# Performance work log

Measured on AMD Instinct MI355X. Metric: run time of the kernel, lower is better.

The kernel has to match this reference:

```python
import jax, jax.numpy as jnp
import numpy as np

EMBED_DIM = 512
NHEAD = 8
HEAD_DIM = EMBED_DIM // NHEAD
NEG_INF = -1e8
U, B, R, S, M = 1024, 16, 256, 32, 31
Q = R + U + S   # 1312
KV = M + R + U  # 1311


def setup_inputs() -> dict:
    key = jax.random.key(0)
    ks = jax.random.split(key, 12)
    f = lambda k, shp: jax.random.normal(k, shp, dtype=jnp.float32)
    s = 1.0 / np.sqrt(EMBED_DIM)
    return {
        "utterance": f(ks[0], (U, B, EMBED_DIM)),
        "right_context": f(ks[1], (R, B, EMBED_DIM)),
        "summary": f(ks[2], (S, B, EMBED_DIM)),
        "memory": f(ks[3], (M, B, EMBED_DIM)),
        "attention_mask": jax.random.randint(ks[4], (Q, KV), 0, 2).astype(bool),
        "padding_mask": jax.random.randint(ks[5], (B, KV), 0, 2).astype(bool),
        "Wq": f(ks[6], (EMBED_DIM, EMBED_DIM)) * s,
        "bq": f(ks[7], (EMBED_DIM,)) * 0.1,
        "Wkv": f(ks[8], (2 * EMBED_DIM, EMBED_DIM)) * s,
        "bkv": f(ks[9], (2 * EMBED_DIM,)) * 0.1,
        "Wo": f(ks[10], (EMBED_DIM, EMBED_DIM)) * s * 0.25,
        "bo": f(ks[11], (EMBED_DIM,)) * 0.1,
    }


def reference(utterance, right_context, summary, memory, attention_mask,
              padding_mask, Wq, bq, Wkv, bkv, Wo, bo):
    scaling = HEAD_DIM ** -0.5
    # query = [right_context, utterance, summary]  -> (Q, B, D)
    q_in = jnp.concatenate([right_context, utterance, summary], axis=0)
    # key/value = [memory, right_context, utterance] -> (KV, B, D)
    kv_in = jnp.concatenate([memory, right_context, utterance], axis=0)
    query = q_in @ Wq.T + bq
    kv = kv_in @ Wkv.T + bkv
    key_t, value = jnp.split(kv, 2, axis=2)

    def heads(t):  # (L, B, D) -> (B*nhead, L, head_dim)
        return t.reshape(t.shape[0], B * NHEAD, HEAD_DIM).transpose(1, 0, 2)

    qh = heads(query) * scaling
    kh = heads(key_t)
    vh = heads(value)
    # (B*nhead, Q, KV) attention scores in float32 (matches .float() cast)
    w = jnp.einsum('bqd,bkd->bqk', qh, kh).astype(jnp.float32)
    w = jnp.where(attention_mask[None], NEG_INF, w)
    w = w.reshape(B, NHEAD, Q, KV)
    w = jnp.where(padding_mask[:, None, None, :], NEG_INF, w)
    probs = jax.nn.softmax(w.reshape(B * NHEAD, Q, KV), axis=-1)
    # dropout p=0.0 -> identity
    attn = jnp.einsum('bqk,bkd->bqd', probs, vh)  # (B*nhead, Q, head_dim)
    attn = attn.transpose(1, 0, 2).reshape(Q, B, EMBED_DIM)
    out = attn @ Wo.T + bo
    output_right_context_utterance = out[:R + U]
    # tanh_on_mem=False -> clamp to [-10, 10]; forward returns memory[:-1]
    output_memory = jnp.clip(out[R + U:], -10.0, 10.0)[:-1]
    return output_right_context_utterance, output_memory
```

## Files before the change

### kernel.cpp

```cpp
#include <hip/hip_runtime.h>
#include <hip/hip_bf16.h>

#define EMBED 512
#define NHEAD 8
#define HDIM  64
#define B_    16
#define U_    1024
#define R_    256
#define S_    32
#define M_    31
#define Q_    (R_ + U_ + S_)
#define KV_   (M_ + R_ + U_)

#define QROWS  (Q_ * B_)
#define KVROWS (KV_ * B_)
#define OROWS  (1311 * B_)
#define OUT0_ROWS (1280 * B_)

#define KVPAD_ROWS 1344
#define KPAD 1344
#define MROWSTRIDE 44

#define QSCALE 0.18033688011112042f
#define SOFF  16.0f
#define MASKV (-40.0f)

typedef __attribute__((ext_vector_type(8))) short bf16x8;
typedef __attribute__((ext_vector_type(4))) short short4v;
typedef __attribute__((ext_vector_type(4))) float f32x4;
#define MFMA16(a, b, c) __builtin_amdgcn_mfma_f32_16x16x32_bf16(a, b, c, 0, 0, 0)

typedef unsigned short ushort_t;

__device__ __forceinline__ ushort_t f2bf(float x) {
    __hip_bfloat16 h = __float2bfloat16(x);
    return *reinterpret_cast<ushort_t*>(&h);
}
__device__ __forceinline__ float bf2f(ushort_t h) {
    return __uint_as_float((unsigned)h << 16);
}
__device__ __forceinline__ float exp2_raw(float x) {
    return __builtin_amdgcn_exp2f(x);
}

__device__ __forceinline__ void gload_lds16(const void* g, void* l) {
    __builtin_amdgcn_global_load_lds(
        (const __attribute__((address_space(1))) unsigned int*)g,
        (__attribute__((address_space(3))) unsigned int*)l, 16, 0, 0);
}

__global__ __launch_bounds__(256) void cvt_all(
    const float* __restrict__ s0, const float* __restrict__ s1,
    const float* __restrict__ s2, const float* __restrict__ s3,
    const float* __restrict__ s4, const float* __restrict__ s5,
    const float* __restrict__ s6,
    ushort_t* __restrict__ SRC_hi, ushort_t* __restrict__ SRC_lo,
    ushort_t* __restrict__ W_hi,  ushort_t* __restrict__ W_lo,
    const int* __restrict__ am, const int* __restrict__ pm,
    unsigned* __restrict__ am_p, unsigned* __restrict__ pm_p)
{
    int bid = blockIdx.x;
    if (bid >= 5884) {
        const int NA = Q_ * MROWSTRIDE;
        const int NP = B_ * MROWSTRIDE;
        int idx = (bid - 5884) * 256 + threadIdx.x;
        if (idx < NA) {
            int q = idx / MROWSTRIDE, w_ = idx % MROWSTRIDE;
            unsigned bits = 0xFFFFFFFFu;
            if (w_ < 41) {
                bits = 0;
                #pragma unroll 4
                for (int i = 0; i < 32; ++i) {
                    int kg = w_ * 32 + i;
                    int v = (kg < KV_) ? am[(size_t)q * KV_ + kg] : 1;
                    bits |= (unsigned)(v != 0) << i;
                }
            }
            am_p[idx] = bits;
        } else if (idx < NA + NP) {
            int j = idx - NA;
            int bb = j / MROWSTRIDE, w_ = j % MROWSTRIDE;
            unsigned bits = 0xFFFFFFFFu;
            if (w_ < 41) {
                bits = 0;
                #pragma unroll 4
                for (int i = 0; i < 32; ++i) {
                    int kg = w_ * 32 + i;
                    int v = (kg < KV_) ? pm[bb * KV_ + kg] : 1;
                    bits |= (unsigned)(v != 0) << i;
                }
            }
            pm_p[j] = bits;
        }
        return;
    }

    const float* src; ushort_t* hi; ushort_t* lo; int n8;
    if (bid < 4096)      { src = s0; hi = SRC_hi;            lo = SRC_lo;            n8 = 1048576; }
    else if (bid < 5120) { src = s1; hi = SRC_hi + 8388608;  lo = SRC_lo + 8388608;  n8 = 262144; bid -= 4096; }
    else if (bid < 5248) { src = s2; hi = SRC_hi + 10485760; lo = SRC_lo + 10485760; n8 = 32768;  bid -= 5120; }
    else if (bid < 5372) { src = s3; hi = SRC_hi + 10747904; lo = SRC_lo + 10747904; n8 = 31744;  bid -= 5248; }
    else if (bid < 5500) { src = s4; hi = W_hi;              lo = W_lo;              n8 = 32768;  bid -= 5372; }
    else if (bid < 5756) { src = s5; hi = W_hi + 262144;     lo = W_lo + 262144;     n8 = 65536;  bid -= 5500; }
    else                 { src = s6; hi = W_hi + 786432;     lo = W_lo + 786432;     n8 = 32768;  bid -= 5756; }

    int i = bid * 256 + threadIdx.x;
    if (i >= n8) return;
    const float4* s = (const float4*)(src + (size_t)i * 8);
    float4 a = s[0], b2 = s[1];
    float xs[8] = {a.x, a.y, a.z, a.w, b2.x, b2.y, b2.z, b2.w};
    bf16x8 hv, lv;
    #pragma unroll
    for (int j = 0; j < 8; ++j) {
        ushort_t hb = f2bf(xs[j]);
        hv[j] = (short)hb;
        lv[j] = (short)f2bf(xs[j] - bf2f(hb));
    }
    *(bf16x8*)(hi + (size_t)i * 8) = hv;
    *(bf16x8*)(lo + (size_t)i * 8) = lv;
}

__global__ __launch_bounds__(256) void vtrans(
    const ushort_t* __restrict__ Vp, ushort_t* __restrict__ VT)
{
    __shared__ ushort_t Lt[64][72];
    const int tid = threadIdx.x;
    const int kt  = blockIdx.x;
    const int bh  = blockIdx.y;
    const int b   = bh >> 3, h = bh & 7;
    const int sub = tid >> 3;
    const int g   = tid & 7;

    #pragma unroll
    for (int p = 0; p < 2; ++p) {
        int k = kt * 64 + p * 32 + sub;
        bf16x8 v;
        if (k < KV_) {
            v = *(const bf16x8*)(Vp + ((size_t)k * B_ + b) * EMBED + h * HDIM + g * 8);
        } else {
            #pragma unroll
            for (int j = 0; j < 8; ++j) v[j] = 0;
        }
        #pragma unroll
        for (int j = 0; j < 8; ++j)
            Lt[g * 8 + j][p * 32 + sub] = (ushort_t)v[j];
    }
    __syncthreads();
    #pragma unroll
    for (int p = 0; p < 2; ++p) {
        int d = p * 32 + sub;
        bf16x8 v = *(const bf16x8*)&Lt[d][g * 8];
        *(bf16x8*)(VT + ((size_t)(bh * 64 + d)) * KPAD + kt * 64 + g * 8) = v;
    }
}

template<int MODE>
__global__ __launch_bounds__(256) void gemm_mfma(
    const ushort_t* __restrict__ Ahi, const ushort_t* __restrict__ Alo,
    const ushort_t* __restrict__ Whi,
    const float* __restrict__ bias, float scale,
    int n0, int n01, int nrows,
    size_t off0, size_t off1, size_t off2,
    void* __restrict__ o0, void* __restrict__ o1, void* __restrict__ o2)
{
    constexpr int TERMS = (MODE == 1) ? 1 : 2;
    __shared__ __align__(16) ushort_t lAhi[128][64];
    __shared__ __align__(16) ushort_t lAlo[(TERMS == 2) ? 128 : 1][64];
    __shared__ __align__(16) ushort_t lWhi[128][64];

    const int tid = threadIdx.x;
    const int w   = tid >> 6;
    const int l   = tid & 63;
    const int l15 = l & 15;
    const int l4  = l >> 4;
    const int row0 = blockIdx.x * 128;
    const int col0 = blockIdx.y * 128;

    const int drow = l >> 3;
    const int sgr  = (l & 7) ^ drow;
    const ushort_t* aptr[4];
    const ushort_t* wptr[4];
    #pragma unroll
    for (int c = 0; c < 4; ++c) {
        int r = row0 + w * 32 + c * 8 + drow;
        int rc = r < nrows ? r : nrows - 1;
        size_t roff;
        if (MODE == 2)      roff = (size_t)rc * EMBED;
        else if (rc < n0)   roff = off0 + (size_t)rc * EMBED;
        else if (rc < n01)  roff = off1 + (size_t)(rc - n0) * EMBED;
        else                roff = off2 + (size_t)(rc - n01) * EMBED;
        aptr[c] = Ahi + roff + sgr * 8;
        int wr = col0 + w * 32 + c * 8 + drow;
        wptr[c] = Whi + (size_t)wr * EMBED + sgr * 8;
    }
    const ptrdiff_t dA = Alo - Ahi;

    f32x4 acc[4][4];
    #pragma unroll
    for (int mi = 0; mi < 4; ++mi)
        #pragma unroll
        for (int nj = 0; nj < 4; ++nj) acc[mi][nj] = (f32x4){0.f, 0.f, 0.f, 0.f};

    const int wrow = (w >> 1) * 64;
    const int wcol = (w & 1) * 64;

    for (int t = 0; t < 8; ++t) {
        __syncthreads();
        const int ke = t * 64;
        #pragma unroll
        for (int c = 0; c < 4; ++c) {
            gload_lds16(aptr[c] + ke, &lAhi[w * 32 + c * 8][0]);
            if (TERMS == 2)
                gload_lds16(aptr[c] + ke + dA, &lAlo[w * 32 + c * 8][0]);
            gload_lds16(wptr[c] + ke, &lWhi[w * 32 + c * 8][0]);
        }
        __syncthreads();

        #pragma unroll
        for (int kk = 0; kk < 2; ++kk) {
            bf16x8 ah[4], al_[4], wh[4];
            #pragma unroll
            for (int mi = 0; mi < 4; ++mi) {
                int row = wrow + mi * 16 + l15;
                int g = (((kk * 4 + l4) ^ (l15 & 7))) * 8;
                ah[mi] = *(const bf16x8*)&lAhi[row][g];
                if (TERMS == 2) al_[mi] = *(const bf16x8*)&lAlo[row][g];
            }
            #pragma unroll
            for (int nj = 0; nj < 4; ++nj) {
                int row = wcol + nj * 16 + l15;
                int g = (((kk * 4 + l4) ^ (l15 & 7))) * 8;
                wh[nj] = *(const bf16x8*)&lWhi[row][g];
            }
            #pragma unroll
            for (int mi = 0; mi < 4; ++mi)
                #pragma unroll
                for (int nj = 0; nj < 4; ++nj) {
                    acc[mi][nj] = MFMA16(ah[mi], wh[nj], acc[mi][nj]);
                    if (TERMS == 2)
                        acc[mi][nj] = MFMA16(al_[mi], wh[nj], acc[mi][nj]);
                }
        }
    }

    #pragma unroll
    for (int nj = 0; nj < 4; ++nj) {
        int gc = col0 + wcol + nj * 16 + l15;
        float bv = bias[gc];
        #pragma unroll
        for (int mi = 0; mi < 4; ++mi) {
            #pragma unroll
            for (int r = 0; r < 4; ++r) {
                int gr = row0 + wrow + mi * 16 + l4 * 4 + r;
                if (gr >= nrows) continue;
                float v = (acc[mi][nj][r] + bv) * scale;
                if (MODE == 0) {
                    ushort_t hb = f2bf(v);
                    ((ushort_t*)o0)[(size_t)gr * EMBED + gc] = hb;
                    ((ushort_t*)o1)[(size_t)gr * EMBED + gc] = f2bf(v - bf2f(hb));
                } else if (MODE == 1) {
                    if (gc < EMBED)
                        ((ushort_t*)o0)[(size_t)gr * EMBED + gc] = f2bf(v);
                    else
                        ((ushort_t*)o2)[(size_t)gr * EMBED + (gc - EMBED)] = f2bf(v);
                } else {
                    if (gr < OUT0_ROWS)
                        ((float*)o0)[(size_t)gr * EMBED + gc] = v;
                    else if (gr < OROWS)
                        ((float*)o1)[(size_t)(gr - OUT0_ROWS) * EMBED + gc] =
                            fminf(fmaxf(v, -10.f), 10.f);
                }
            }
        }
    }
}

__global__ __launch_bounds__(512, 4) void attn_mfma(
    const ushort_t* __restrict__ Qhi_p, const ushort_t* __restrict__ Qlo_p,
    const ushort_t* __restrict__ Khi_p, const ushort_t* __restrict__ VT,
    const unsigned* __restrict__ am_p, const unsigned* __restrict__ pm_p,
    ushort_t* __restrict__ Chi_p, ushort_t* __restrict__ Clo_p)
{
    __shared__ __align__(16) ushort_t Kl[2][64][64];
    __shared__ __align__(16) ushort_t Vt[2][64][64];
    __shared__ __align__(16) ushort_t Pb[8][16][72];

    const int tid = threadIdx.x;
    const int w   = tid >> 6;
    const int l   = tid & 63;
    const int l15 = l & 15;
    const int l4  = l >> 4;
    const int q0  = blockIdx.x * 128;
    const int bh  = blockIdx.y;
    const int b   = bh >> 3, h = bh & 7;

    bf16x8 Qhi[2], Qlo[2];
    {
        int qa = q0 + w * 16 + l15;
        if (qa >= Q_) qa = Q_ - 1;
        size_t base = ((size_t)qa * B_ + b) * EMBED + h * HDIM;
        #pragma unroll
        for (int dh = 0; dh < 2; ++dh) {
            Qhi[dh] = *(const bf16x8*)(Qhi_p + base + dh * 32 + l4 * 8);
            Qlo[dh] = *(const bf16x8*)(Qlo_p + base + dh * 32 + l4 * 8);
        }
    }

    bf16x8 ONES;
    #pragma unroll
    for (int j = 0; j < 8; ++j) ONES[j] = (l15 == 0) ? (short)0x3F80 : (short)0;

    const unsigned* awp;
    {
        int q = q0 + w * 16 + l15;
        if (q >= Q_) q = Q_ - 1;
        awp = am_p + (size_t)q * MROWSTRIDE;
    }
    const unsigned* pwp = pm_p + b * MROWSTRIDE;

    const int krl  = l >> 3;
    const int gsrc = (l & 7) ^ krl;
    const int srow = w * 8 + krl;

    const ushort_t* kSrc0 =
        Khi_p + ((size_t)srow * B_ + b) * EMBED + h * HDIM + gsrc * 8;
    const ushort_t* vSrc0 =
        VT + ((size_t)(bh * 64 + srow)) * KPAD + gsrc * 8;

    f32x4 SS = (f32x4){0.f, 0.f, 0.f, 0.f};
    f32x4 O[4];
    #pragma unroll
    for (int dg = 0; dg < 4; ++dg) O[dg] = (f32x4){0.f, 0.f, 0.f, 0.f};

    auto stage = [&](int kbase, int buf) {
        gload_lds16(kSrc0 + (size_t)kbase * B_ * EMBED, &Kl[buf][w * 8][0]);
        gload_lds16(vSrc0 + kbase, &Vt[buf][w * 8][0]);
    };

    stage(0, 0);
    __syncthreads();
    int cur = 0;

    for (int kt = 0; kt < 21; ++kt) {
        uint2 pw  = *(const uint2*)&pwp[2 * kt];
        uint2 awv = *(const uint2*)&awp[2 * kt];
        unsigned m0 = (awv.x | pw.x) >> (l4 * 4);
        unsigned m1 = (awv.y | pw.y) >> (l4 * 4);

        if (kt < 20) stage((kt + 1) * 64, cur ^ 1);

        f32x4 S[4];
        __builtin_amdgcn_s_setprio(1);
        #pragma unroll
        for (int c = 0; c < 4; ++c) {
            f32x4 acc = (f32x4){0.f, 0.f, 0.f, 0.f};
            int krow = c * 16 + l15;
            #pragma unroll
            for (int dh = 0; dh < 2; ++dh) {
                int gr = ((dh * 4 + l4) ^ (krow & 7)) * 8;
                bf16x8 Bh = *(const bf16x8*)&Kl[cur][krow][gr];
                acc = MFMA16(Bh, Qhi[dh], acc);
                acc = MFMA16(Bh, Qlo[dh], acc);
            }
            S[c] = acc;
        }
        __builtin_amdgcn_s_setprio(0);

        #pragma unroll
        for (int c = 0; c < 4; ++c) {
            unsigned mw = (c & 2) ? m1 : m0;
            int sh = (c & 1) << 4;
            short4v pk;
            #pragma unroll
            for (int r = 0; r < 4; ++r) {
                float s = ((mw >> (sh + r)) & 1) ? MASKV : S[c][r];
                pk[r] = (short)f2bf(exp2_raw(s - SOFF));
            }
            *(short4v*)&Pb[w][l15][c * 16 + l4 * 4] = pk;
        }

        bf16x8 PA[2];
        #pragma unroll
        for (int kh = 0; kh < 2; ++kh)
            PA[kh] = *(const bf16x8*)&Pb[w][l15][kh * 32 + l4 * 8];

        __builtin_amdgcn_s_setprio(1);
        SS = MFMA16(PA[0], ONES, SS);
        SS = MFMA16(PA[1], ONES, SS);
        #pragma unroll
        for (int kh = 0; kh < 2; ++kh)
            #pragma unroll
            for (int dg = 0; dg < 4; ++dg) {
                int vcb = ((kh * 4 + l4) ^ (l15 & 7)) << 3;
                bf16x8 VB = *(const bf16x8*)&Vt[cur][dg * 16 + l15][vcb];
                O[dg] = MFMA16(PA[kh], VB, O[dg]);
            }
        __builtin_amdgcn_s_setprio(0);

        __syncthreads();
        cur ^= 1;
    }

    #pragma unroll
    for (int r = 0; r < 4; ++r) {
        int qd = q0 + w * 16 + l4 * 4 + r;
        if (qd >= Q_) continue;
        float sT = __shfl(SS[r], l & 48, 64);
        float inv = 1.f / sT;
        #pragma unroll
        for (int dg = 0; dg < 4; ++dg) {
            float v = O[dg][r] * inv;
            size_t off = ((size_t)qd * B_ + b) * EMBED + h * HDIM + dg * 16 + l15;
            ushort_t hb = f2bf(v);
            Chi_p[off] = hb;
            Clo_p[off] = f2bf(v - bf2f(hb));
        }
    }
}

extern "C" void kernel_launch(void* const* d_in, const int* in_sizes, int n_in,
                              void* d_out, int out_size, void* d_ws, size_t ws_size,
                              hipStream_t stream) {
    const float* utter = (const float*)d_in[0];
    const float* rctx  = (const float*)d_in[1];
    const float* summ  = (const float*)d_in[2];
    const float* mem   = (const float*)d_in[3];
    const int* amask   = (const int*)d_in[4];
    const int* pmask   = (const int*)d_in[5];
    const float* Wq  = (const float*)d_in[6];
    const float* bq  = (const float*)d_in[7];
    const float* Wkv = (const float*)d_in[8];
    const float* bkv = (const float*)d_in[9];
    const float* Wo  = (const float*)d_in[10];
    const float* bo  = (const float*)d_in[11];

    const size_t UT_OFF = 0;
    const size_t RC_OFF = 8388608;
    const size_t SM_OFF = 10485760;
    const size_t MM_OFF = 10747904;
    const size_t SRC_N  = 11001856;
    const size_t WQ_OFF = 0, WKV_OFF = 262144, WO_OFF = 786432;
    const size_t W_N = 1048576;
    const size_t KVPLANE = (size_t)KVPAD_ROWS * B_ * EMBED;

    ushort_t* p = (ushort_t*)d_ws;
    ushort_t* SRC_hi = p;                p += SRC_N;
    ushort_t* SRC_lo = p;                p += SRC_N;
    ushort_t* Wp_hi  = p;                p += W_N;
    ushort_t* Wp_lo  = p;                p += W_N;
    ushort_t* Qhi_p  = p;                p += (size_t)QROWS * EMBED;
    ushort_t* Qlo_p  = p;                p += (size_t)QROWS * EMBED;
    ushort_t* Khi_p  = p;                p += KVPLANE;
    ushort_t* VT_p   = p;                p += KVPLANE;
    ushort_t* Vp     = p;                p += KVPLANE;
    ushort_t* Chi_p  = p;                p += (size_t)QROWS * EMBED;
    ushort_t* Clo_p  = p;                p += (size_t)QROWS * EMBED;
    unsigned* am_p   = (unsigned*)p;     p += (size_t)2 * KVPAD_ROWS * MROWSTRIDE;
    unsigned* pm_p   = (unsigned*)p;     p += (size_t)2 * B_ * MROWSTRIDE;

    float* out0 = (float*)d_out;
    float* out1 = out0 + (size_t)OUT0_ROWS * EMBED;

    dim3 blk(256);

    cvt_all<<<dim3(6113), blk, 0, stream>>>(
        utter, rctx, summ, mem, Wq, Wkv, Wo,
        SRC_hi, SRC_lo, Wp_hi, Wp_lo,
        amask, pmask, am_p, pm_p);

    gemm_mfma<0><<<dim3(QROWS / 128, EMBED / 128), blk, 0, stream>>>(
        SRC_hi, SRC_lo, Wp_hi + WQ_OFF, bq, QSCALE,
        R_ * B_, (R_ + U_) * B_, QROWS, RC_OFF, UT_OFF, SM_OFF,
        Qhi_p, Qlo_p, nullptr);

    gemm_mfma<1><<<dim3((KVROWS + 127) / 128, (2 * EMBED) / 128), blk, 0, stream>>>(
        SRC_hi, SRC_lo, Wp_hi + WKV_OFF, bkv, 1.0f,
        M_ * B_, (M_ + R_) * B_, KVROWS, MM_OFF, RC_OFF, UT_OFF,
        Khi_p, nullptr, Vp);

    vtrans<<<dim3(21, 128), blk, 0, stream>>>(Vp, VT_p);

    attn_mfma<<<dim3((Q_ + 127) / 128, B_ * NHEAD), dim3(512), 0, stream>>>(
        Qhi_p, Qlo_p, Khi_p, VT_p, am_p, pm_p, Chi_p, Clo_p);

    gemm_mfma<2><<<dim3(QROWS / 128, EMBED / 128), blk, 0, stream>>>(
        Chi_p, Clo_p, Wp_hi + WO_OFF, bo, 1.0f,
        QROWS, QROWS, QROWS, 0, 0, 0,
        out0, out1, nullptr);
}
```

Baseline: 334.1 us.

## Keep attention probabilities in registers by transposing MFMA operand roles

The attention kernel no longer writes the softmax probabilities to shared memory and reads them back. It swaps the MFMA operand order so the P fragment produced in registers can feed the PV and row-sum MFMAs directly. The V transpose kernel pre-permutes half-groups so the new operand layout can be read with swizzled 8-byte loads. The epilogue stages the output tile through the reused shared buffer so global stores are coalesced per row. In exchange, V fragment loads become two narrower LDS reads, and the permutation couples the layout tightly across both kernels.

```diff
diff --git a/kernel.cpp b/kernel.cpp
--- a/kernel.cpp
+++ b/kernel.cpp
@@ -150,6 +150,12 @@
     for (int p = 0; p < 2; ++p) {
         int d = p * 32 + sub;
         bf16x8 v = *(const bf16x8*)&Lt[d][g * 8];
+        if (d & 8) {
+            bf16x8 t;
+            #pragma unroll
+            for (int j = 0; j < 8; ++j) t[j] = v[j ^ 4];
+            v = t;
+        }
         *(bf16x8*)(VT + ((size_t)(bh * 64 + d)) * KPAD + kt * 64 + g * 8) = v;
     }
 }
@@ -281,9 +287,9 @@
     const unsigned* __restrict__ am_p, const unsigned* __restrict__ pm_p,
     ushort_t* __restrict__ Chi_p, ushort_t* __restrict__ Clo_p)
 {
-    __shared__ __align__(16) ushort_t Kl[2][64][64];
-    __shared__ __align__(16) ushort_t Vt[2][64][64];
-    __shared__ __align__(16) ushort_t Pb[8][16][72];
+    __shared__ __align__(16) ushort_t SM[16384];
+    #define KlAt(buf, row) (SM + (buf) * 4096 + (row) * 64)
+    #define VtAt(buf, row) (SM + 8192 + (buf) * 4096 + (row) * 64)
 
     const int tid = threadIdx.x;
     const int w   = tid >> 6;
@@ -327,14 +333,18 @@
     const ushort_t* vSrc0 =
         VT + ((size_t)(bh * 64 + srow)) * KPAD + gsrc * 8;
 
+    const int gb  = l4 >> 1;
+    const int hsw = ((l4 & 1) ^ ((l15 >> 3) & 1)) * 4;
+    const int x7  = l15 & 7;
+
     f32x4 SS = (f32x4){0.f, 0.f, 0.f, 0.f};
     f32x4 O[4];
     #pragma unroll
     for (int dg = 0; dg < 4; ++dg) O[dg] = (f32x4){0.f, 0.f, 0.f, 0.f};
 
     auto stage = [&](int kbase, int buf) {
-        gload_lds16(kSrc0 + (size_t)kbase * B_ * EMBED, &Kl[buf][w * 8][0]);
-        gload_lds16(vSrc0 + kbase, &Vt[buf][w * 8][0]);
+        gload_lds16(kSrc0 + (size_t)kbase * B_ * EMBED, KlAt(buf, w * 8));
+        gload_lds16(vSrc0 + kbase, VtAt(buf, w * 8));
     };
 
     stage(0, 0);
@@ -358,7 +368,7 @@
             #pragma unroll
             for (int dh = 0; dh < 2; ++dh) {
                 int gr = ((dh * 4 + l4) ^ (krow & 7)) * 8;
-                bf16x8 Bh = *(const bf16x8*)&Kl[cur][krow][gr];
+                bf16x8 Bh = *(const bf16x8*)(KlAt(cur, krow) + gr);
                 acc = MFMA16(Bh, Qhi[dh], acc);
                 acc = MFMA16(Bh, Qlo[dh], acc);
             }
@@ -366,56 +376,66 @@
         }
         __builtin_amdgcn_s_setprio(0);
 
+        bf16x8 PB[2];
         #pragma unroll
         for (int c = 0; c < 4; ++c) {
             unsigned mw = (c & 2) ? m1 : m0;
             int sh = (c & 1) << 4;
-            short4v pk;
             #pragma unroll
             for (int r = 0; r < 4; ++r) {
                 float s = ((mw >> (sh + r)) & 1) ? MASKV : S[c][r];
-                pk[r] = (short)f2bf(exp2_raw(s - SOFF));
-            }
-            *(short4v*)&Pb[w][l15][c * 16 + l4 * 4] = pk;
-        }
-
-        bf16x8 PA[2];
-        #pragma unroll
-        for (int kh = 0; kh < 2; ++kh)
-            PA[kh] = *(const bf16x8*)&Pb[w][l15][kh * 32 + l4 * 8];
+                PB[c >> 1][(c & 1) * 4 + r] = (short)f2bf(exp2_raw(s - SOFF));
+            }
+        }
 
         __builtin_amdgcn_s_setprio(1);
-        SS = MFMA16(PA[0], ONES, SS);
-        SS = MFMA16(PA[1], ONES, SS);
-        #pragma unroll
-        for (int kh = 0; kh < 2; ++kh)
+        SS = MFMA16(ONES, PB[0], SS);
+        SS = MFMA16(ONES, PB[1], SS);
+        #pragma unroll
+        for (int kh = 0; kh < 2; ++kh) {
             #pragma unroll
             for (int dg = 0; dg < 4; ++dg) {
-                int vcb = ((kh * 4 + l4) ^ (l15 & 7)) << 3;
-                bf16x8 VB = *(const bf16x8*)&Vt[cur][dg * 16 + l15][vcb];
-                O[dg] = MFMA16(PA[kh], VB, O[dg]);
-            }
+                int rw = dg * 16 + l15;
+                const ushort_t* vrow = VtAt(cur, rw);
+                int G0 = (kh * 4 + gb) ^ x7;
+                int G1 = (kh * 4 + 2 + gb) ^ x7;
+                union { bf16x8 v8; short4v h2[2]; } u;
+                u.h2[0] = *(const short4v*)(vrow + G0 * 8 + hsw);
+                u.h2[1] = *(const short4v*)(vrow + G1 * 8 + hsw);
+                O[dg] = MFMA16(u.v8, PB[kh], O[dg]);
+            }
+        }
         __builtin_amdgcn_s_setprio(0);
 
         __syncthreads();
         cur ^= 1;
     }
 
-    #pragma unroll
-    for (int r = 0; r < 4; ++r) {
-        int qd = q0 + w * 16 + l4 * 4 + r;
-        if (qd >= Q_) continue;
-        float sT = __shfl(SS[r], l & 48, 64);
-        float inv = 1.f / sT;
-        #pragma unroll
-        for (int dg = 0; dg < 4; ++dg) {
-            float v = O[dg][r] * inv;
-            size_t off = ((size_t)qd * B_ + b) * EMBED + h * HDIM + dg * 16 + l15;
-            ushort_t hb = f2bf(v);
-            Chi_p[off] = hb;
-            Clo_p[off] = f2bf(v - bf2f(hb));
-        }
-    }
+    float sT  = __shfl(SS[0], l15, 64);
+    float inv = 1.f / sT;
+
+    float* TB = ((float*)SM) + w * 1024;
+    #pragma unroll
+    for (int dg = 0; dg < 4; ++dg) {
+        f32x4 vv;
+        #pragma unroll
+        for (int r = 0; r < 4; ++r) vv[r] = O[dg][r] * inv;
+        int gsw = (dg * 4 + l4) ^ (l15 & 7);
+        *(f32x4*)(TB + l15 * 64 + gsw * 4) = vv;
+    }
+
+    #pragma unroll
+    for (int qq = 0; qq < 16; ++qq) {
+        int q = q0 + w * 16 + qq;
+        if (q >= Q_) break;
+        float v = TB[qq * 64 + (((l >> 2) ^ (qq & 7)) * 4) + (l & 3)];
+        size_t off = ((size_t)q * B_ + b) * EMBED + h * HDIM + l;
+        ushort_t hb = f2bf(v);
+        Chi_p[off] = hb;
+        Clo_p[off] = f2bf(v - bf2f(hb));
+    }
+    #undef KlAt
+    #undef VtAt
 }
 
 extern "C" void kernel_launch(void* const* d_in, const int* in_sizes, int n_in,
```

Result: no change. 336.7 us (+0.8%).
